# Performance work log

Measured on AMD Instinct MI355X. Metric: run time of the kernel, lower is better.

## Reference

```python
import jax, jax.numpy as jnp
import numpy as np

R = 0.2                 # radius (init kwarg r)
MAX_NEIGHBORS = 32      # init kwarg max_num_neighbors
N = 16384
N_BATCH = 8


def setup_inputs() -> dict:
    key = jax.random.key(0)
    k1, k2, k3, k4 = jax.random.split(key, 4)
    node_coord_src = jax.random.uniform(k1, (N, 3), dtype=jnp.float32)
    node_coord_dst = jax.random.uniform(k2, (N, 3), dtype=jnp.float32)
    batch_src = jnp.sort(jax.random.randint(k3, (N,), 0, N_BATCH, dtype=jnp.int64))
    batch_dst = jnp.sort(jax.random.randint(k4, (N,), 0, N_BATCH, dtype=jnp.int64))
    return {
        "node_coord_src": node_coord_src,
        "batch_src": batch_src,
        "node_coord_dst": node_coord_dst,
        "batch_dst": batch_dst,
    }


def reference(node_coord_src, batch_src, node_coord_dst, batch_dst):
    """Batch-aware radius graph: for each dst point, up to MAX_NEIGHBORS src
    points within radius R and in the same batch (deterministically the
    lowest-index ones). Returns fixed-shape padded (edge_src, edge_dst),
    padded with -1 where fewer than MAX_NEIGHBORS neighbors exist."""
    n_src = node_coord_src.shape[0]
    n_dst = node_coord_dst.shape[0]

    # squared pairwise distances [n_dst, n_src] without [N,N,3] intermediate
    s2 = jnp.sum(node_coord_src * node_coord_src, axis=-1)          # [n_src]
    d2 = jnp.sum(node_coord_dst * node_coord_dst, axis=-1)          # [n_dst]
    cross = jnp.einsum("nd,md->nm", node_coord_dst, node_coord_src)  # [n_dst,n_src]
    dist2 = d2[:, None] + s2[None, :] - 2.0 * cross

    valid = (dist2 <= R * R) & (batch_dst[:, None] == batch_src[None, :])

    # pick first MAX_NEIGHBORS valid src indices per dst: encode src index,
    # invalid -> n_src (sentinel), take K smallest via top_k of negation
    src_idx = jnp.arange(n_src, dtype=jnp.int32)
    keyed = jnp.where(valid, src_idx[None, :], n_src)               # [n_dst,n_src]
    neg_sel, _ = jax.lax.top_k(-keyed, MAX_NEIGHBORS)
    sel = -neg_sel                                                  # [n_dst,K]
    found = sel < n_src

    edge_src = jnp.where(found, sel, -1)
    edge_dst = jnp.where(found, jnp.arange(n_dst, dtype=jnp.int32)[:, None], -1)
    return edge_src.reshape(-1), edge_dst.reshape(-1)
```

## Files before the change

kernel.cpp:

```cpp
#include <hip/hip_runtime.h>

#define K 32
#define NB 8

__global__ void bounds_kernel(const int* __restrict__ batch_src, int n_src,
                              int* __restrict__ bounds) {
    const int b = threadIdx.x;
    if (b > NB) return;
    int lo = 0, hi = n_src;
    while (lo < hi) {
        int mid = (lo + hi) >> 1;
        if (batch_src[mid] < b) lo = mid + 1; else hi = mid;
    }
    bounds[b] = lo;
}

__global__ __launch_bounds__(256) void RadiusConnect_kernel(
    const float* __restrict__ src_xyz,
    const float* __restrict__ dst_xyz, const int* __restrict__ batch_dst,
    const int* __restrict__ bounds,
    int n_dst, int* __restrict__ out)
{
    const int wave = (blockIdx.x * blockDim.x + threadIdx.x) >> 6;
    const int lane = threadIdx.x & 63;
    if (wave >= n_dst) return;
    const int d = wave;

    const float xd = dst_xyz[3 * d + 0];
    const float yd = dst_xyz[3 * d + 1];
    const float zd = dst_xyz[3 * d + 2];
    const float d2 = __fadd_rn(__fadd_rn(__fmul_rn(xd, xd), __fmul_rn(yd, yd)),
                               __fmul_rn(zd, zd));
    const int b = batch_dst[d];
    const int start = bounds[b];
    const int end   = bounds[b + 1];

    const float rr = __fmul_rn(0.2f, 0.2f);
    int* __restrict__ out_src = out;
    int* __restrict__ out_dst = out + (size_t)n_dst * K;
    const long long base = (long long)d * K;
    const unsigned long long lt_mask = (1ull << lane) - 1ull;

    int count = 0;
    for (int j0 = start; j0 < end && count < K; j0 += 256) {
        float xs[4], ys[4], zs[4];
        int jj[4];
#pragma unroll
        for (int g = 0; g < 4; ++g) {
            int j = j0 + g * 64 + lane;
            jj[g] = j;
            int jl = j < end ? j : end - 1;
            xs[g] = src_xyz[3 * jl + 0];
            ys[g] = src_xyz[3 * jl + 1];
            zs[g] = src_xyz[3 * jl + 2];
        }
        bool valid[4];
#pragma unroll
        for (int g = 0; g < 4; ++g) {
            const float s2 = __fadd_rn(
                __fadd_rn(__fmul_rn(xs[g], xs[g]), __fmul_rn(ys[g], ys[g])),
                __fmul_rn(zs[g], zs[g]));
            const float cross = __fadd_rn(
                __fadd_rn(__fmul_rn(xd, xs[g]), __fmul_rn(yd, ys[g])),
                __fmul_rn(zd, zs[g]));
            const float dist2 = __fsub_rn(__fadd_rn(d2, s2),
                                          __fmul_rn(2.0f, cross));
            valid[g] = (jj[g] < end) && (dist2 <= rr);
        }
#pragma unroll
        for (int g = 0; g < 4; ++g) {
            const unsigned long long mask = __ballot(valid[g]);
            const int rank = count + __popcll(mask & lt_mask);
            if (valid[g] && rank < K) {
                out_src[base + rank] = jj[g];
                out_dst[base + rank] = d;
            }
            count += __popcll(mask);
        }
    }

    if (count < K && lane >= count && lane < K) {
        out_src[base + lane] = -1;
        out_dst[base + lane] = -1;
    }
}

extern "C" void kernel_launch(void* const* d_in, const int* in_sizes, int n_in,
                              void* d_out, int out_size, void* d_ws, size_t ws_size,
                              hipStream_t stream) {
    const float* src_xyz   = (const float*)d_in[0];
    const int*   batch_src = (const int*)d_in[1];
    const float* dst_xyz   = (const float*)d_in[2];
    const int*   batch_dst = (const int*)d_in[3];
    int* out    = (int*)d_out;
    int* bounds = (int*)d_ws;

    const int n_src = in_sizes[0] / 3;
    const int n_dst = in_sizes[2] / 3;

    bounds_kernel<<<1, 16, 0, stream>>>(batch_src, n_src, bounds);

    const int threads = 256;
    const int blocks = (n_dst * 64 + threads - 1) / threads;
    RadiusConnect_kernel<<<blocks, threads, 0, stream>>>(
        src_xyz, dst_xyz, batch_dst, bounds, n_dst, out);
}
```

Measured before the change: 87.09 us.

## Pack source points as float4 with precomputed norm and prefetch next tile

A setup kernel now packs each source point into a float4 holding x, y, z and the squared norm, and also computes the batch bounds. The main kernel loads one 16-byte vector per point instead of three strided scalars, skips recomputing s2, and double-buffers the next 256-point chunk while it tests the current one. This costs an extra pass over the sources, more workspace, and extra registers for the prefetch buffers, and the prefetched chunk is wasted when a wave exits early after finding K neighbours.

```diff
diff --git a/kernel.cpp b/kernel.cpp
--- a/kernel.cpp
+++ b/kernel.cpp
@@ -3,20 +3,31 @@
 #define K 32
 #define NB 8
 
-__global__ void bounds_kernel(const int* __restrict__ batch_src, int n_src,
-                              int* __restrict__ bounds) {
-    const int b = threadIdx.x;
-    if (b > NB) return;
-    int lo = 0, hi = n_src;
-    while (lo < hi) {
-        int mid = (lo + hi) >> 1;
-        if (batch_src[mid] < b) lo = mid + 1; else hi = mid;
+__global__ void setup_kernel(const float* __restrict__ src_xyz,
+                             const int* __restrict__ batch_src, int n_src,
+                             int* __restrict__ bounds,
+                             float4* __restrict__ packed) {
+    const int i = blockIdx.x * blockDim.x + threadIdx.x;
+    if (i < n_src) {
+        const float x = src_xyz[3 * i + 0];
+        const float y = src_xyz[3 * i + 1];
+        const float z = src_xyz[3 * i + 2];
+        const float s2 = __fadd_rn(__fadd_rn(__fmul_rn(x, x), __fmul_rn(y, y)),
+                                   __fmul_rn(z, z));
+        packed[i] = make_float4(x, y, z, s2);
     }
-    bounds[b] = lo;
+    if (i <= NB) {
+        int lo = 0, hi = n_src;
+        while (lo < hi) {
+            int mid = (lo + hi) >> 1;
+            if (batch_src[mid] < i) lo = mid + 1; else hi = mid;
+        }
+        bounds[i] = lo;
+    }
 }
 
 __global__ __launch_bounds__(256) void RadiusConnect_kernel(
-    const float* __restrict__ src_xyz,
+    const float4* __restrict__ src_p,
     const float* __restrict__ dst_xyz, const int* __restrict__ batch_dst,
     const int* __restrict__ bounds,
     int n_dst, int* __restrict__ out)
@@ -39,43 +50,51 @@
     int* __restrict__ out_src = out;
     int* __restrict__ out_dst = out + (size_t)n_dst * K;
     const long long base = (long long)d * K;
-    const unsigned long long lt_mask = (1ull << lane) - 1ull;
+    const unsigned long long lt = (1ull << lane) - 1ull;
 
     int count = 0;
-    for (int j0 = start; j0 < end && count < K; j0 += 256) {
-        float xs[4], ys[4], zs[4];
-        int jj[4];
+    if (start < end) {
+        const int last = end - 1;
+        float4 cur[4], nxt[4];
 #pragma unroll
         for (int g = 0; g < 4; ++g) {
-            int j = j0 + g * 64 + lane;
-            jj[g] = j;
-            int jl = j < end ? j : end - 1;
-            xs[g] = src_xyz[3 * jl + 0];
-            ys[g] = src_xyz[3 * jl + 1];
-            zs[g] = src_xyz[3 * jl + 2];
+            const int j = start + g * 64 + lane;
+            cur[g] = src_p[j < last ? j : last];
         }
-        bool valid[4];
+        int j0 = start;
+        while (true) {
+            const int jn = j0 + 256;
+            const bool more = (jn < end);
+            if (more) {
 #pragma unroll
-        for (int g = 0; g < 4; ++g) {
-            const float s2 = __fadd_rn(
-                __fadd_rn(__fmul_rn(xs[g], xs[g]), __fmul_rn(ys[g], ys[g])),
-                __fmul_rn(zs[g], zs[g]));
-            const float cross = __fadd_rn(
-                __fadd_rn(__fmul_rn(xd, xs[g]), __fmul_rn(yd, ys[g])),
-                __fmul_rn(zd, zs[g]));
-            const float dist2 = __fsub_rn(__fadd_rn(d2, s2),
-                                          __fmul_rn(2.0f, cross));
-            valid[g] = (jj[g] < end) && (dist2 <= rr);
-        }
+                for (int g = 0; g < 4; ++g) {
+                    const int j = jn + g * 64 + lane;
+                    nxt[g] = src_p[j < last ? j : last];
+                }
+            }
 #pragma unroll
-        for (int g = 0; g < 4; ++g) {
-            const unsigned long long mask = __ballot(valid[g]);
-            const int rank = count + __popcll(mask & lt_mask);
-            if (valid[g] && rank < K) {
-                out_src[base + rank] = jj[g];
-                out_dst[base + rank] = d;
+            for (int g = 0; g < 4; ++g) {
+                const int j = j0 + g * 64 + lane;
+                const float xs = cur[g].x, ys = cur[g].y, zs = cur[g].z;
+                const float s2 = cur[g].w;
+                const float cross = __fadd_rn(
+                    __fadd_rn(__fmul_rn(xd, xs), __fmul_rn(yd, ys)),
+                    __fmul_rn(zd, zs));
+                const float dist2 = __fsub_rn(__fadd_rn(d2, s2),
+                                              __fmul_rn(2.0f, cross));
+                const bool valid = (j <= last) && (dist2 <= rr);
+                const unsigned long long m = __ballot(valid);
+                const int rank = count + __popcll(m & lt);
+                if (valid && rank < K) {
+                    out_src[base + rank] = j;
+                    out_dst[base + rank] = d;
+                }
+                count += __popcll(m);
             }
-            count += __popcll(mask);
+            if (count >= K || !more) break;
+            j0 = jn;
+#pragma unroll
+            for (int g = 0; g < 4; ++g) cur[g] = nxt[g];
         }
     }
 
@@ -92,16 +111,19 @@
     const int*   batch_src = (const int*)d_in[1];
     const float* dst_xyz   = (const float*)d_in[2];
     const int*   batch_dst = (const int*)d_in[3];
-    int* out    = (int*)d_out;
-    int* bounds = (int*)d_ws;
+    int* out = (int*)d_out;
+
+    int*    bounds = (int*)d_ws;
+    float4* packed = (float4*)((char*)d_ws + 256);
 
     const int n_src = in_sizes[0] / 3;
     const int n_dst = in_sizes[2] / 3;
 
-    bounds_kernel<<<1, 16, 0, stream>>>(batch_src, n_src, bounds);
+    setup_kernel<<<(n_src + 255) / 256, 256, 0, stream>>>(
+        src_xyz, batch_src, n_src, bounds, packed);
 
     const int threads = 256;
     const int blocks = (n_dst * 64 + threads - 1) / threads;
     RadiusConnect_kernel<<<blocks, threads, 0, stream>>>(
-        src_xyz, dst_xyz, batch_dst, bounds, n_dst, out);
+        packed, dst_xyz, batch_dst, bounds, n_dst, out);
 }
```

Result: no change. 87.70 us (+0.7%).

## Record ballot masks in shared memory and emit coalesced outputs after scan

Applied to the files above, without the earlier changes.

The scan loop now handles 64 source points per iteration instead of 256. Each non-empty ballot mask and its base index are saved to per-wave shared memory, and the per-chunk scattered writes are removed. After the scan, each of the first 32 lanes finds its rank's chunk, selects the bit position by binary popcount search, and writes its output slot in one coalesced store that also covers padding. This cuts loads issued past the point where 32 neighbors are found and removes divergent scattered stores. In exchange it adds a serial loop over up to 40 saved masks and less load-level parallelism per iteration.

```diff
diff --git a/kernel.cpp b/kernel.cpp
--- a/kernel.cpp
+++ b/kernel.cpp
@@ -2,6 +2,7 @@
 
 #define K 32
 #define NB 8
+#define MAXM 40
 
 __global__ void bounds_kernel(const int* __restrict__ batch_src, int n_src,
                               int* __restrict__ bounds) {
@@ -15,73 +16,84 @@
     bounds[b] = lo;
 }
 
-__global__ __launch_bounds__(256) void RadiusConnect_kernel(
+__global__ __launch_bounds__(256) void radius_kernel(
     const float* __restrict__ src_xyz,
     const float* __restrict__ dst_xyz, const int* __restrict__ batch_dst,
-    const int* __restrict__ bounds,
-    int n_dst, int* __restrict__ out)
+    const int* __restrict__ bounds, int n_dst, int* __restrict__ out)
 {
-    const int wave = (blockIdx.x * blockDim.x + threadIdx.x) >> 6;
+    __shared__ unsigned long long s_mask[4][MAXM];
+    __shared__ int                s_base[4][MAXM];
+
+    const int w    = threadIdx.x >> 6;
     const int lane = threadIdx.x & 63;
-    if (wave >= n_dst) return;
-    const int d = wave;
+    const int d    = (blockIdx.x * blockDim.x + threadIdx.x) >> 6;
+    if (d >= n_dst) return;
 
     const float xd = dst_xyz[3 * d + 0];
     const float yd = dst_xyz[3 * d + 1];
     const float zd = dst_xyz[3 * d + 2];
     const float d2 = __fadd_rn(__fadd_rn(__fmul_rn(xd, xd), __fmul_rn(yd, yd)),
                                __fmul_rn(zd, zd));
-    const int b = batch_dst[d];
+    const int b     = batch_dst[d];
     const int start = bounds[b];
     const int end   = bounds[b + 1];
 
-    const float rr = __fmul_rn(0.2f, 0.2f);
-    int* __restrict__ out_src = out;
-    int* __restrict__ out_dst = out + (size_t)n_dst * K;
-    const long long base = (long long)d * K;
-    const unsigned long long lt_mask = (1ull << lane) - 1ull;
+    int count = 0;
+    int nm    = 0;
 
-    int count = 0;
-    for (int j0 = start; j0 < end && count < K; j0 += 256) {
-        float xs[4], ys[4], zs[4];
-        int jj[4];
-#pragma unroll
-        for (int g = 0; g < 4; ++g) {
-            int j = j0 + g * 64 + lane;
-            jj[g] = j;
-            int jl = j < end ? j : end - 1;
-            xs[g] = src_xyz[3 * jl + 0];
-            ys[g] = src_xyz[3 * jl + 1];
-            zs[g] = src_xyz[3 * jl + 2];
-        }
-        bool valid[4];
-#pragma unroll
-        for (int g = 0; g < 4; ++g) {
-            const float s2 = __fadd_rn(
-                __fadd_rn(__fmul_rn(xs[g], xs[g]), __fmul_rn(ys[g], ys[g])),
-                __fmul_rn(zs[g], zs[g]));
-            const float cross = __fadd_rn(
-                __fadd_rn(__fmul_rn(xd, xs[g]), __fmul_rn(yd, ys[g])),
-                __fmul_rn(zd, zs[g]));
-            const float dist2 = __fsub_rn(__fadd_rn(d2, s2),
-                                          __fmul_rn(2.0f, cross));
-            valid[g] = (jj[g] < end) && (dist2 <= rr);
-        }
-#pragma unroll
-        for (int g = 0; g < 4; ++g) {
-            const unsigned long long mask = __ballot(valid[g]);
-            const int rank = count + __popcll(mask & lt_mask);
-            if (valid[g] && rank < K) {
-                out_src[base + rank] = jj[g];
-                out_dst[base + rank] = d;
-            }
-            count += __popcll(mask);
+    for (int j0 = start; j0 < end && count < K; j0 += 64) {
+        const int j  = j0 + lane;
+        const int jc = j < end ? j : end - 1;
+        const float xs = src_xyz[3 * jc + 0];
+        const float ys = src_xyz[3 * jc + 1];
+        const float zs = src_xyz[3 * jc + 2];
+        const float s2 = __fadd_rn(
+            __fadd_rn(__fmul_rn(xs, xs), __fmul_rn(ys, ys)),
+            __fmul_rn(zs, zs));
+        const float cross = __fadd_rn(
+            __fadd_rn(__fmul_rn(xd, xs), __fmul_rn(yd, ys)),
+            __fmul_rn(zd, zs));
+        const float dist2 = __fsub_rn(__fadd_rn(d2, s2),
+                                      __fmul_rn(2.0f, cross));
+        const bool valid = (j < end) && (dist2 <= 0.04f);
+        const unsigned long long m = __ballot(valid);
+        if (m != 0ull && nm < MAXM) {
+            if (lane == 0) { s_mask[w][nm] = m; s_base[w][nm] = j0; }
+            count += __popcll(m);
+            ++nm;
         }
     }
 
-    if (count < K && lane >= count && lane < K) {
-        out_src[base + lane] = -1;
-        out_dst[base + lane] = -1;
+    const long long obase = (long long)d * K;
+    if (lane < K) {
+        int rem = lane;
+        unsigned long long x = 0ull;
+        int jb = 0;
+        bool found = false;
+        for (int q = 0; q < nm; ++q) {
+            const unsigned long long mq = s_mask[w][q];
+            const int c = __popcll(mq);
+            const bool here = (!found) && (rem < c);
+            if (here) { x = mq; jb = s_base[w][q]; }
+            if (!found && !here) rem -= c;
+            found = found || here;
+        }
+        int val = -1;
+        if (found) {
+            int pos = 0;
+            unsigned y;
+            int c = __popcll(x & 0xFFFFFFFFull);
+            if (rem >= c) { rem -= c; y = (unsigned)(x >> 32); pos = 32; }
+            else          { y = (unsigned)x; }
+            c = __popc(y & 0xFFFFu); if (rem >= c) { rem -= c; y >>= 16; pos += 16; }
+            c = __popc(y & 0xFFu);   if (rem >= c) { rem -= c; y >>= 8;  pos += 8;  }
+            c = __popc(y & 0xFu);    if (rem >= c) { rem -= c; y >>= 4;  pos += 4;  }
+            c = __popc(y & 0x3u);    if (rem >= c) { rem -= c; y >>= 2;  pos += 2;  }
+            c = (int)(y & 1u);       if (rem >= c) { pos += 1; }
+            val = jb + pos;
+        }
+        out[obase + lane] = val;
+        out[(long long)n_dst * K + obase + lane] = found ? d : -1;
     }
 }
 
@@ -102,6 +114,6 @@
 
     const int threads = 256;
     const int blocks = (n_dst * 64 + threads - 1) / threads;
-    RadiusConnect_kernel<<<blocks, threads, 0, stream>>>(
+    radius_kernel<<<blocks, threads, 0, stream>>>(
         src_xyz, dst_xyz, batch_dst, bounds, n_dst, out);
 }
```

After: 94.36 us. +8.3%, slower.
